# Optimization experiments

Hardware: AMD Instinct MI355X
Metric: run time of the kernel (lower is better)

## Reference

```python
import jax, jax.numpy as jnp
import numpy as np

D_MODEL = 4096
D_FF = 11008
W_SCALE = 0.02  # keep activations in a sane range


def setup_inputs() -> dict:
    key = jax.random.key(0)
    k1, k2, k3, k4 = jax.random.split(key, 4)
    x = jax.random.normal(k1, (1, 1, D_MODEL), dtype=jnp.float32)
    Wup = jax.random.normal(k2, (D_FF, D_MODEL), dtype=jnp.float32) * W_SCALE
    Wgatet = jax.random.normal(k3, (D_MODEL, D_FF), dtype=jnp.float32) * W_SCALE
    Wdownt = jax.random.normal(k4, (D_FF, D_MODEL), dtype=jnp.float32) * W_SCALE
    threshold = jnp.float32(0.1)
    return {"x": x, "Wup": Wup, "Wgatet": Wgatet, "Wdownt": Wdownt,
            "threshold": threshold}


def reference(x, Wup, Wgatet, Wdownt, threshold):
    # x: [B, S, d]; Wup: [d_ff, d]; Wgatet: [d, d_ff]; Wdownt: [d_ff, d]
    if x.shape[0] == 1 and x.shape[1] == 1:
        # decode path: threshold-flagged activation sparsity
        x1 = jax.nn.silu(jnp.matmul(x, Wgatet))          # [1,1,d_ff]
        flags = jnp.abs(x1) > threshold                   # [1,1,d_ff] bool
        # gather_gemv_elemul_flag_3d: only flagged rows of Wup contribute
        z = jnp.where(flags, jnp.matmul(x, Wup.T) * x1, 0.0)  # [1,1,d_ff]
        # gather_transposed_gemv_flag_3d: only flagged rows of Wdownt contribute
        return jnp.matmul(z, Wdownt)                      # [1,1,d]
    # prefill path: dense SwiGLU
    z = jnp.matmul(x, Wup.T) * jax.nn.silu(jnp.matmul(x, Wgatet))
    return jnp.matmul(z, Wdownt)
```

## Files before the change

kernel.cpp:

```cpp
#include <hip/hip_runtime.h>
#include <hip/hip_bf16.h>
#include <math.h>

#define D_MODEL 4096
#define D_FF    11008
#define F4      (D_FF / 4)
#define D4      (D_MODEL / 4)

#define K1_ROWS   32
#define K1_CHUNKS (D_MODEL / K1_ROWS)
#define K3_BLOCKS 256
#define K3_ROWS   (D_FF / K3_BLOCKS)

__global__ __launch_bounds__(256) void gate_part_k(const float* __restrict__ x,
                                                   const float* __restrict__ Wg,
                                                   float* __restrict__ gpart) {
    const int j4  = blockIdx.x * 256 + threadIdx.x;
    const bool act = (j4 < F4);
    const int i0  = blockIdx.y * K1_ROWS;
    const float4* __restrict__ W4 = (const float4*)Wg;

    float4 acc = make_float4(0.f, 0.f, 0.f, 0.f);
    for (int i = i0; i < i0 + K1_ROWS; i += 4) {
        const float4 xv = *(const float4*)(x + i);
        if (act) {
            float4 w;
            w = W4[(size_t)(i + 0) * F4 + j4];
            acc.x += xv.x * w.x; acc.y += xv.x * w.y; acc.z += xv.x * w.z; acc.w += xv.x * w.w;
            w = W4[(size_t)(i + 1) * F4 + j4];
            acc.x += xv.y * w.x; acc.y += xv.y * w.y; acc.z += xv.y * w.z; acc.w += xv.y * w.w;
            w = W4[(size_t)(i + 2) * F4 + j4];
            acc.x += xv.z * w.x; acc.y += xv.z * w.y; acc.z += xv.z * w.z; acc.w += xv.z * w.w;
            w = W4[(size_t)(i + 3) * F4 + j4];
            acc.x += xv.w * w.x; acc.y += xv.w * w.y; acc.z += xv.w * w.z; acc.w += xv.w * w.w;
        }
    }
    if (act)
        *(float4*)(gpart + (size_t)blockIdx.y * D_FF + 4 * (size_t)j4) = acc;
}

__global__ __launch_bounds__(256) void up_gemv_k(const float* __restrict__ x,
                                                 const float* __restrict__ Wup,
                                                 const float* __restrict__ gpart,
                                                 const float* __restrict__ thr_p,
                                                 float* __restrict__ z) {
    const int wave = threadIdx.x >> 6;
    const int lane = threadIdx.x & 63;
    const int j = blockIdx.x * 4 + wave;

    float r = gpart[(size_t)lane * D_FF + j] + gpart[(size_t)(lane + 64) * D_FF + j];
#pragma unroll
    for (int off = 32; off > 0; off >>= 1)
        r += __shfl_xor(r, off);

    const float x1  = r / (1.0f + __expf(-r));
    const float thr = *thr_p;

    if (!(fabsf(x1) > thr)) {
        if (lane == 0) z[j] = 0.0f;
        return;
    }

    const float4* __restrict__ A = (const float4*)(Wup + (size_t)j * D_MODEL);
    const float4* __restrict__ X = (const float4*)x;
    float acc = 0.0f;
#pragma unroll
    for (int k = 0; k < 16; ++k) {
        const float4 a  = A[k * 64 + lane];
        const float4 xv = X[k * 64 + lane];
        acc += a.x * xv.x + a.y * xv.y + a.z * xv.z + a.w * xv.w;
    }
#pragma unroll
    for (int off = 32; off > 0; off >>= 1)
        acc += __shfl_down(acc, off);

    if (lane == 0) z[j] = acc * x1;
}

__global__ __launch_bounds__(512) void down_part_k(const float* __restrict__ z,
                                                   const float* __restrict__ Wd,
                                                   float* __restrict__ dpart) {
    const int t  = threadIdx.x;
    const int j0 = blockIdx.x * K3_ROWS;
    const float4* __restrict__ W4 = (const float4*)Wd;

    float4 a0 = make_float4(0.f, 0.f, 0.f, 0.f);
    float4 a1 = make_float4(0.f, 0.f, 0.f, 0.f);

    for (int r = 0; r < K3_ROWS; ++r) {
        const int j = j0 + r;
        const float zj = z[j];
        if (zj != 0.0f) {
            const float4 w0 = W4[(size_t)j * D4 + t];
            const float4 w1 = W4[(size_t)j * D4 + 512 + t];
            a0.x += zj * w0.x; a0.y += zj * w0.y; a0.z += zj * w0.z; a0.w += zj * w0.w;
            a1.x += zj * w1.x; a1.y += zj * w1.y; a1.z += zj * w1.z; a1.w += zj * w1.w;
        }
    }
    float4* dp = (float4*)dpart + (size_t)blockIdx.x * D4;
    dp[t]       = a0;
    dp[512 + t] = a1;
}

__global__ __launch_bounds__(256) void down_reduce_k(const float* __restrict__ dpart,
                                                     float* __restrict__ out) {
    const int t     = threadIdx.x;
    const int col   = (t & 31);
    const int slice = (t >> 5);
    const int c4    = blockIdx.x * 32 + col;

    const float4* __restrict__ dp = (const float4*)dpart;
    float4 acc = make_float4(0.f, 0.f, 0.f, 0.f);
    for (int s = 0; s < 32; ++s) {
        const int b = slice * 32 + s;
        const float4 v = dp[(size_t)b * D4 + c4];
        acc.x += v.x; acc.y += v.y; acc.z += v.z; acc.w += v.w;
    }

    __shared__ float4 red[256];
    red[t] = acc;
    __syncthreads();
    if (t < 32) {
        float4 r = red[t];
#pragma unroll
        for (int s = 1; s < 8; ++s) {
            const float4 v = red[t + 32 * s];
            r.x += v.x; r.y += v.y; r.z += v.z; r.w += v.w;
        }
        ((float4*)out)[c4] = r;
    }
}

extern "C" void kernel_launch(void* const* d_in, const int* in_sizes, int n_in,
                              void* d_out, int out_size, void* d_ws, size_t ws_size,
                              hipStream_t stream) {
    const float* x    = (const float*)d_in[0];
    const float* Wup  = (const float*)d_in[1];
    const float* Wg   = (const float*)d_in[2];
    const float* Wd   = (const float*)d_in[3];
    const float* thr  = (const float*)d_in[4];
    float* out = (float*)d_out;

    float* gpart = (float*)d_ws;
    float* z     = gpart + (size_t)K1_CHUNKS * D_FF;
    float* dpart = z + D_FF;

    gate_part_k<<<dim3(11, K1_CHUNKS), 256, 0, stream>>>(x, Wg, gpart);

    up_gemv_k<<<D_FF / 4, 256, 0, stream>>>(x, Wup, gpart, thr, z);

    down_part_k<<<K3_BLOCKS, 512, 0, stream>>>(z, Wd, dpart);

    down_reduce_k<<<D4 / 32, 256, 0, stream>>>(dpart, out);
}
```

Baseline: 468.9 us.

## Reshape gate and down GEMV grids and drop zero-row skip in down projection

The gate partial-sum kernel now uses 64-row chunks, so the up kernel reads one partial per lane instead of two. The down projection is re-gridded from 256 large blocks over row slices to a 2D grid of column tiles by 64-row chunks. Its inner loop is now branch-free and unrolled, so more loads can be in flight. In exchange it reads every Wdownt row, including rows whose z is zero, which adds memory traffic for the rows that sparsity used to skip. The reduce kernel is adjusted to sum the new number of partial chunks with a strided loop.

```diff
diff --git a/kernel.cpp b/kernel.cpp
--- a/kernel.cpp
+++ b/kernel.cpp
@@ -7,23 +7,23 @@
 #define F4      (D_FF / 4)
 #define D4      (D_MODEL / 4)
 
-#define K1_ROWS   32
-#define K1_CHUNKS (D_MODEL / K1_ROWS)
-#define K3_BLOCKS 256
-#define K3_ROWS   (D_FF / K3_BLOCKS)
+#define G_CHUNK   64
+#define G_NCHUNK  (D_MODEL / G_CHUNK)
+#define DN_ROWS   64
+#define DN_NCHUNK (D_FF / DN_ROWS)
 
 __global__ __launch_bounds__(256) void gate_part_k(const float* __restrict__ x,
                                                    const float* __restrict__ Wg,
                                                    float* __restrict__ gpart) {
-    const int j4  = blockIdx.x * 256 + threadIdx.x;
-    const bool act = (j4 < F4);
-    const int i0  = blockIdx.y * K1_ROWS;
+    const int j4 = blockIdx.x * 256 + threadIdx.x;
+    const int i0 = blockIdx.y * G_CHUNK;
     const float4* __restrict__ W4 = (const float4*)Wg;
 
-    float4 acc = make_float4(0.f, 0.f, 0.f, 0.f);
-    for (int i = i0; i < i0 + K1_ROWS; i += 4) {
-        const float4 xv = *(const float4*)(x + i);
-        if (act) {
+    if (j4 < F4) {
+        float4 acc = make_float4(0.f, 0.f, 0.f, 0.f);
+#pragma unroll 4
+        for (int i = i0; i < i0 + G_CHUNK; i += 4) {
+            const float4 xv = *(const float4*)(x + i);
             float4 w;
             w = W4[(size_t)(i + 0) * F4 + j4];
             acc.x += xv.x * w.x; acc.y += xv.x * w.y; acc.z += xv.x * w.z; acc.w += xv.x * w.w;
@@ -34,9 +34,8 @@
             w = W4[(size_t)(i + 3) * F4 + j4];
             acc.x += xv.w * w.x; acc.y += xv.w * w.y; acc.z += xv.w * w.z; acc.w += xv.w * w.w;
         }
+        *(float4*)(gpart + (size_t)blockIdx.y * D_FF + 4 * (size_t)j4) = acc;
     }
-    if (act)
-        *(float4*)(gpart + (size_t)blockIdx.y * D_FF + 4 * (size_t)j4) = acc;
 }
 
 __global__ __launch_bounds__(256) void up_gemv_k(const float* __restrict__ x,
@@ -48,7 +47,7 @@
     const int lane = threadIdx.x & 63;
     const int j = blockIdx.x * 4 + wave;
 
-    float r = gpart[(size_t)lane * D_FF + j] + gpart[(size_t)(lane + 64) * D_FF + j];
+    float r = gpart[(size_t)lane * D_FF + j];
 #pragma unroll
     for (int off = 32; off > 0; off >>= 1)
         r += __shfl_xor(r, off);
@@ -77,29 +76,22 @@
     if (lane == 0) z[j] = acc * x1;
 }
 
-__global__ __launch_bounds__(512) void down_part_k(const float* __restrict__ z,
+__global__ __launch_bounds__(256) void down_part_k(const float* __restrict__ z,
                                                    const float* __restrict__ Wd,
                                                    float* __restrict__ dpart) {
-    const int t  = threadIdx.x;
-    const int j0 = blockIdx.x * K3_ROWS;
+    const int c4 = blockIdx.x * 256 + threadIdx.x;
+    const int j0 = blockIdx.y * DN_ROWS;
     const float4* __restrict__ W4 = (const float4*)Wd;
 
-    float4 a0 = make_float4(0.f, 0.f, 0.f, 0.f);
-    float4 a1 = make_float4(0.f, 0.f, 0.f, 0.f);
-
-    for (int r = 0; r < K3_ROWS; ++r) {
+    float4 acc = make_float4(0.f, 0.f, 0.f, 0.f);
+#pragma unroll 8
+    for (int r = 0; r < DN_ROWS; ++r) {
         const int j = j0 + r;
-        const float zj = z[j];
-        if (zj != 0.0f) {
-            const float4 w0 = W4[(size_t)j * D4 + t];
-            const float4 w1 = W4[(size_t)j * D4 + 512 + t];
-            a0.x += zj * w0.x; a0.y += zj * w0.y; a0.z += zj * w0.z; a0.w += zj * w0.w;
-            a1.x += zj * w1.x; a1.y += zj * w1.y; a1.z += zj * w1.z; a1.w += zj * w1.w;
-        }
+        const float  zj = z[j];
+        const float4 w  = W4[(size_t)j * D4 + c4];
+        acc.x += zj * w.x; acc.y += zj * w.y; acc.z += zj * w.z; acc.w += zj * w.w;
     }
-    float4* dp = (float4*)dpart + (size_t)blockIdx.x * D4;
-    dp[t]       = a0;
-    dp[512 + t] = a1;
+    ((float4*)dpart)[(size_t)blockIdx.y * D4 + c4] = acc;
 }
 
 __global__ __launch_bounds__(256) void down_reduce_k(const float* __restrict__ dpart,
@@ -111,8 +103,7 @@
 
     const float4* __restrict__ dp = (const float4*)dpart;
     float4 acc = make_float4(0.f, 0.f, 0.f, 0.f);
-    for (int s = 0; s < 32; ++s) {
-        const int b = slice * 32 + s;
+    for (int b = slice; b < DN_NCHUNK; b += 8) {
         const float4 v = dp[(size_t)b * D4 + c4];
         acc.x += v.x; acc.y += v.y; acc.z += v.z; acc.w += v.w;
     }
@@ -142,14 +133,14 @@
     float* out = (float*)d_out;
 
     float* gpart = (float*)d_ws;
-    float* z     = gpart + (size_t)K1_CHUNKS * D_FF;
+    float* z     = gpart + (size_t)G_NCHUNK * D_FF;
     float* dpart = z + D_FF;
 
-    gate_part_k<<<dim3(11, K1_CHUNKS), 256, 0, stream>>>(x, Wg, gpart);
+    gate_part_k<<<dim3(11, G_NCHUNK), 256, 0, stream>>>(x, Wg, gpart);
 
     up_gemv_k<<<D_FF / 4, 256, 0, stream>>>(x, Wup, gpart, thr, z);
 
-    down_part_k<<<K3_BLOCKS, 512, 0, stream>>>(z, Wd, dpart);
+    down_part_k<<<dim3(4, DN_NCHUNK), 256, 0, stream>>>(z, Wd, dpart);
 
     down_reduce_k<<<D4 / 32, 256, 0, stream>>>(dpart, out);
 }
```

After: 468.5 us. About the same (-0.1%).
